# Kernel tuning notes

Hardware: AMD Instinct MI355X
Metric: run time of the kernel (lower is better)

## Reference

```python
import jax, jax.numpy as jnp
import numpy as np

EPS = 1e-9
TAU = 100.0
HX = 1.0
HY = 1.0


def _sym_pad(x):
    # torch Pad(1, padding_mode='symmetric') == numpy/jnp 'symmetric'
    return jnp.pad(x, ((0, 0), (0, 0), (1, 1), (1, 1)), mode='symmetric')


def _zero_interior(x):
    # zeroPadGS: keep interior, zero 1-px border
    return jnp.pad(x[:, :, 1:-1, 1:-1], ((0, 0), (0, 0), (1, 1), (1, 1)))


def _frob(x):
    # per-(batch,channel) Frobenius norm; only used in control-flow comparisons
    return jax.lax.stop_gradient(jnp.sqrt(jnp.sum(x * x, axis=(2, 3))))


def _apply_stencil(inp, boo, bmo, bom, bop, bpo):
    # applyStencilGS: mirror-pad interior, apply 5-point stencil, zero border
    p = _sym_pad(inp[:, :, 1:-1, 1:-1])
    res = (boo * p[:, :, 1:-1, 1:-1]
           + bmo * p[:, :, :-2, 1:-1]
           + bom * p[:, :, 1:-1, :-2]
           + bop * p[:, :, 1:-1, 2:]
           + bpo * p[:, :, 2:, 1:-1])
    return jnp.pad(res, ((0, 0), (0, 0), (1, 1), (1, 1)))


def _forward(V, mask1, mask2, kmax):
    B, C, nx0, ny0 = V.shape
    # U = per-image mean of V
    U = jnp.broadcast_to(jnp.mean(V, axis=(2, 3), keepdims=True), V.shape)
    Ut = jnp.swapaxes(_sym_pad(U), 2, 3)
    Vt = jnp.swapaxes(_sym_pad(V), 2, 3)
    m1 = jnp.swapaxes(_sym_pad(mask1), 2, 3)
    m2 = jnp.swapaxes(_sym_pad(mask2), 2, 3)
    nx, ny = ny0, nx0
    # drift vectors: forward difference / forward average (conv f1/f2, f3/f4)
    d1 = (Vt[:, :, 1:, :] - Vt[:, :, :-1, :]) / (HX * 0.5 * (Vt[:, :, 1:, :] + Vt[:, :, :-1, :]))
    d2 = (Vt[:, :, :, 1:] - Vt[:, :, :, :-1]) / (HY * 0.5 * (Vt[:, :, :, 1:] + Vt[:, :, :, :-1]))
    d1f = jnp.zeros_like(Vt).at[:, :, :nx + 1, 1:ny + 1].set(d1[:, :, :, 1:ny + 1]) * m1
    d2f = jnp.zeros_like(Vt).at[:, :, 1:nx + 1, :ny + 1].set(d2[:, :, 1:nx + 1, :]) * m2
    rx, ry = TAU / (2 * HX), TAU / (2 * HY)
    rxx, ryy = TAU / (HX * HX), TAU / (HY * HY)
    # conv 'same' with kernel [1,-1,0] (cross-correlation): out[i] = d[i-1] - d[i]
    c1 = jnp.pad(d1f, ((0, 0), (0, 0), (1, 0), (0, 0)))[:, :, :-1, :] - d1f
    c2 = jnp.pad(d2f, ((0, 0), (0, 0), (0, 0), (1, 0)))[:, :, :, :-1] - d2f
    boo_full = 1 + 2 * (rxx + ryy) - rx * c1 - ry * c2
    boo = boo_full[:, :, 1:nx + 1, 1:ny + 1]
    bpo = -rxx + rx * d1f[:, :, 1:nx + 1, 1:ny + 1]
    bop = -ryy + ry * d2f[:, :, 1:nx + 1, 1:ny + 1]
    bmo = -rxx - rx * d1f[:, :, :nx, 1:ny + 1]
    bom = -ryy - ry * d2f[:, :, 1:nx + 1, :ny]

    A = lambda z: _apply_stencil(z, boo, bmo, bom, bop, bpo)
    thresh = EPS * nx * ny
    x0 = Ut
    b = Ut
    p0 = _zero_interior(b - A(x0))
    r0_abs = _frob(p0)
    zc = jnp.zeros((B, C), dtype=V.dtype)
    zf = jnp.zeros_like(x0)
    k0 = jnp.zeros((B, C), dtype=jnp.int32)
    carry0 = (x0, p0, p0, zf, p0, zf, zf, zf, r0_abs, r0_abs, zc, zc, zc, zc, zc, k0)

    def step(carry, _):
        x, r, r_0, r_old, p, v, s, t, r_abs, r0_abs, sigma, alpha, omega, beta, v_abs, k = carry
        conv = (k < kmax) & (r_abs > thresh)
        convE = conv[:, :, None, None]
        v = jnp.where(convE, A(p), v)
        sigma = jnp.where(conv, jnp.sum(v * r_0, axis=(2, 3)), sigma)
        v_abs = jnp.where(conv, _frob(v), v_abs)
        res = sigma <= EPS * v_abs * r0_abs
        res1 = conv & res
        res1E = res1[:, :, None, None]
        p = jnp.where(res1E, _zero_interior(b - A(x)), p)
        r = jnp.where(res1E, p, r)
        r_0 = jnp.where(res1E, p, r_0)
        r0_abs = jnp.where(res1, _frob(r_0), r0_abs)
        r_abs = jnp.where(res1, r0_abs, r_abs)
        k = jnp.where(res1, k + 1, k)
        nres = conv & ~res
        nresE = nres[:, :, None, None]
        alpha = jnp.where(nres, jnp.sum(r * r_0, axis=(2, 3)) / jnp.where(nres, sigma, 1.0), alpha)
        s = jnp.where(nresE, r - alpha[:, :, None, None] * v, s)
        conv2 = _frob(s) <= thresh
        c3E = (nres & conv2)[:, :, None, None]
        x = jnp.where(c3E, x + alpha[:, :, None, None] * p, x)
        r = jnp.where(c3E, s, r)
        c4 = nres & ~conv2
        c4E = c4[:, :, None, None]
        t = jnp.where(c4E, A(s), t)
        omega = jnp.where(c4, jnp.sum(t * s, axis=(2, 3)) / jnp.where(c4, jnp.sum(t * t, axis=(2, 3)), 1.0), omega)
        x = jnp.where(c4E, x + alpha[:, :, None, None] * p + omega[:, :, None, None] * s, x)
        r_old = jnp.where(c4E, r, r_old)
        r = jnp.where(c4E, s - omega[:, :, None, None] * t, r)
        beta = jnp.where(c4, (alpha / jnp.where(c4, omega, 1.0)) * (jnp.sum(r * r_0, axis=(2, 3)) / jnp.where(c4, jnp.sum(r_old * r_0, axis=(2, 3)), 1.0)), beta)
        p = jnp.where(c4E, r + beta[:, :, None, None] * (p - omega[:, :, None, None] * v), p)
        k = jnp.where(nres, k + 1, k)
        r_abs = jnp.where(nres, _frob(r), r_abs)
        return (x, r, r_0, r_old, p, v, s, t, r_abs, r0_abs, sigma, alpha, omega, beta, v_abs, k), None

    carry, _ = jax.lax.scan(step, carry0, jnp.arange(kmax))
    return carry[0]


def setup_inputs() -> dict:
    key = jax.random.key(0)
    k1, k2, k3 = jax.random.split(key, 3)
    B, C, N = 8, 1, 512
    # strictly positive guidance image (V + offset in the original)
    V = jax.random.uniform(k1, (B, C, N, N), dtype=jnp.float32) * 0.99 + 0.005
    mask1 = (jax.random.uniform(k2, (B, C, N, N)) < 0.1).astype(jnp.float32)
    mask2 = (jax.random.uniform(k3, (B, C, N, N)) < 0.1).astype(jnp.float32)
    return {"V": V, "mask1": mask1, "mask2": mask2, "kmax": 16}


def reference(V, mask1, mask2, kmax):
    return _forward(V, mask1, mask2, kmax)
```

## Files before the change

kernel.cpp:

```cpp
#include <hip/hip_runtime.h>
#include <math.h>


namespace {

typedef unsigned long long ull;

constexpr int NIMG = 8;
constexpr int NSd  = 512;
constexpr int S    = NSd*NSd;
constexpr int NSF  = NIMG*S;
constexpr int PADS = 514;
constexpr int NB   = 256;
constexpr int IPB  = 32;
constexpr int NT   = 512;
constexpr float EPSF = 1e-9f;
constexpr float THR  = 1e-9f * 262144.0f;
constexpr float RX_=50.f, RY_=50.f, RXX_=100.f, RYY_=100.f;
constexpr float BOO0 = 1.f + 2.f*(RXX_+RYY_);

enum { P_PH=0, P_VH, P_TH, NPLH };
constexpr size_t A_QW = (size_t)NIMG*2*8*32;
constexpr size_t B_QW = (size_t)NIMG*2*8;

__device__ __forceinline__ int cl(int i){ return i<0?0:(i>NSd-1?NSd-1:i); }

#define LD4(d, p) { float4 _t4 = *reinterpret_cast<const float4*>(p); \
  (d)[0]=_t4.x; (d)[1]=_t4.y; (d)[2]=_t4.z; (d)[3]=_t4.w; }
#define ST4(p, s) { *reinterpret_cast<float4*>(p) = \
  make_float4((s)[0],(s)[1],(s)[2],(s)[3]); }
#define CP4(d, s) { (d)[0]=(s)[0]; (d)[1]=(s)[1]; (d)[2]=(s)[2]; (d)[3]=(s)[3]; }

#define LOADCOEF(rr_) \
  float ax[4], by[4], bym[4], axl; \
  LD4(ax, &axp[rr_][c4o]); \
  LD4(by, &byp[rr_][c4o]); \
  axl = __shfl_up(ax[3], 1); \
  if (lane==0) axl = c4o ? axp[rr_][c4o-1] : 0.f; \
  if ((rr_) > 0){ LD4(bym, &byp[(rr_)-1][c4o]); } else { CP4(bym, bym0_); }

__device__ __forceinline__ void hstore4(ull* pq, int off_f, const float s[4]){
  size_t q = (size_t)off_f >> 1;
  ull u0 = ((ull)__float_as_uint(s[1])<<32) | (ull)__float_as_uint(s[0]);
  ull u1 = ((ull)__float_as_uint(s[3])<<32) | (ull)__float_as_uint(s[2]);
  __hip_atomic_store(pq+q,   u0, __ATOMIC_RELAXED, __HIP_MEMORY_SCOPE_AGENT);
  __hip_atomic_store(pq+q+1, u1, __ATOMIC_RELAXED, __HIP_MEMORY_SCOPE_AGENT);
}
__device__ __forceinline__ void hload4(const ull* pq, int off_f, float d[4]){
  size_t q = (size_t)off_f >> 1;
  ull u0 = __hip_atomic_load(pq+q,   __ATOMIC_RELAXED, __HIP_MEMORY_SCOPE_AGENT);
  ull u1 = __hip_atomic_load(pq+q+1, __ATOMIC_RELAXED, __HIP_MEMORY_SCOPE_AGENT);
  d[0]=__uint_as_float((unsigned)u0); d[1]=__uint_as_float((unsigned)(u0>>32));
  d[2]=__uint_as_float((unsigned)u1); d[3]=__uint_as_float((unsigned)(u1>>32));
}

__device__ __forceinline__ void phase_sync(ull* Aq, ull* Bq, int img, int sub,
    unsigned ep, float* v, int n){
  __shared__ float acc[8][5];
  __shared__ float bc[5];
  const int tid = threadIdx.x, w = tid>>6, lane = tid&63;
  #pragma unroll
  for (int i=0;i<5;++i){
    if (i<n){
      float a = v[i];
      #pragma unroll
      for (int o=32;o;o>>=1) a += __shfl_xor(a,o);
      if (lane==0) acc[w][i] = a;
    }
  }
  __syncthreads();
  const int par = ep & 1;
  ull* Ab = Aq + ((size_t)(img*2+par)*8)*32;
  ull* Bb = Bq + ((size_t)(img*2+par))*8;
  if (sub == 0){
    if (w < n){
      float own = 0.f;
      #pragma unroll
      for (int i=0;i<8;++i) own += acc[i][w];
      ull x = 0; const bool me = (lane>=1 && lane<32);
      for(;;){
        bool ok = true;
        if (me){
          x = __hip_atomic_load(Ab + w*32 + lane, __ATOMIC_RELAXED, __HIP_MEMORY_SCOPE_AGENT);
          ok = ((unsigned)x == ep);
        }
        if (__all(ok)) break;
        __builtin_amdgcn_s_sleep(1);
      }
      float a = me ? __uint_as_float((unsigned)(x>>32)) : ((lane==0)? own : 0.f);
      #pragma unroll
      for (int o=16;o;o>>=1) a += __shfl_xor(a,o);
      if (lane==0){
        bc[w] = a;
        ull pk = ((ull)__float_as_uint(a)<<32) | (ull)ep;
        __hip_atomic_store(Bb + w, pk, __ATOMIC_RELAXED, __HIP_MEMORY_SCOPE_AGENT);
      }
    }
  } else {
    if (tid < n){
      float t = 0.f;
      #pragma unroll
      for (int i=0;i<8;++i) t += acc[i][tid];
      ull pk = ((ull)__float_as_uint(t)<<32) | (ull)ep;
      __hip_atomic_store(Ab + tid*32 + sub, pk, __ATOMIC_RELAXED, __HIP_MEMORY_SCOPE_AGENT);
    }
    if (w == 0){
      ull x = 0; const bool me = (lane < n);
      for(;;){
        bool ok = true;
        if (me){
          x = __hip_atomic_load(Bb + lane, __ATOMIC_RELAXED, __HIP_MEMORY_SCOPE_AGENT);
          ok = ((unsigned)x == ep);
        }
        if (__all(ok)) break;
        __builtin_amdgcn_s_sleep(1);
      }
      if (me) bc[lane] = __uint_as_float((unsigned)(x>>32));
    }
  }
  __syncthreads();
  #pragma unroll
  for (int i=0;i<5;++i) if (i<n) v[i] = bc[i];
}

__device__ __forceinline__ void stencil_reg(const float zc[4], float zl, float zr,
    const float zu[4], const float zd[4],
    const float ax[4], float axl, const float by[4], const float bym[4],
    float out[4]){
  #pragma unroll
  for (int j=0;j<4;++j){
    float axm = j ? ax[j-1] : axl;
    float zxm = j ? zc[j-1] : zl;
    float zxp = (j<3) ? zc[j+1] : zr;
    float boo = BOO0 + ax[j] - axm + by[j] - bym[j];
    out[j] = boo*zc[j] + (-RXX_-axm)*zxm + (-RYY_-bym[j])*zu[j]
           + (-RYY_+by[j])*zd[j] + (-RXX_+ax[j])*zxp;
  }
}

__global__ void __launch_bounds__(NT)
solve(const float* __restrict__ Vg,
    const float* __restrict__ M1g, const float* __restrict__ M2g,
    const int* __restrict__ kmp, float* __restrict__ outg, float* __restrict__ ws){
  __shared__ float tile[18][NSd];
  __shared__ float r0l[16][NSd];
  __shared__ float axp[16][NSd];
  __shared__ float byp[16][NSd];
  const int tid = threadIdx.x, blk = blockIdx.x;
  const int img = blk & 7, sub = blk >> 3;
  const int y0 = sub*16, bS = img*S;
  const int cg = tid & 127, r0b = tid >> 7, c4o = cg*4;
  const int lane = tid & 63;
  ull* PHq = (ull*)(ws + (size_t)P_PH*NSF);
  ull* VHq = (ull*)(ws + (size_t)P_VH*NSF);
  ull* THq = (ull*)(ws + (size_t)P_TH*NSF);
  ull* Aq  = (ull*)(ws + (size_t)NPLH*NSF);
  ull* Bq  = Aq + A_QW;
  unsigned ep = 0;
  const int kmax = kmp[0];
  const int row0o  = bS + (y0<<9) + c4o;
  const int row15o = bS + ((y0+15)<<9) + c4o;
  const int rowm1o = bS + ((y0-1)<<9) + c4o;
  const int row16o = bS + ((y0+16)<<9) + c4o;
  float red[5];

  float bym0_[4];
  float msum = 0.f;
  #pragma unroll
  for (int k=0;k<4;++k){
    int rr = 4*r0b + k, fy = y0 + rr, ro = bS + (fy<<9);
    float vc[4], vd[4], m1[4], m2[4], ca[4], cb[4];
    LD4(vc, Vg+ro+c4o);
    float vr  = Vg[ro + (c4o<508 ? c4o+4 : 511)];
    LD4(vd, Vg + bS + (cl(fy+1)<<9) + c4o);
    LD4(m1, M1g+ro+c4o);
    LD4(m2, M2g+ro+c4o);
    #pragma unroll
    for (int j=0;j<4;++j){
      float vn = (j<3) ? vc[j+1] : vr;
      ca[j] = RX_*((vn-vc[j])/(0.5f*(vn+vc[j])))*m1[j];
      cb[j] = RY_*((vd[j]-vc[j])/(0.5f*(vd[j]+vc[j])))*m2[j];
      msum += vc[j];
    }
    ST4(&axp[rr][c4o], ca);
    ST4(&byp[rr][c4o], cb);
  }
  if (r0b==0 && sub>0){
    int ro = bS + (y0<<9);
    float vc[4], vu[4], m2u[4];
    LD4(vc, Vg+ro+c4o);
    LD4(vu, Vg + bS + ((y0-1)<<9) + c4o);
    LD4(m2u, M2g + bS + ((y0-1)<<9) + c4o);
    #pragma unroll
    for (int j=0;j<4;++j)
      bym0_[j] = RY_*((vc[j]-vu[j])/(0.5f*(vc[j]+vu[j])))*m2u[j];
  } else {
    bym0_[0]=0.f; bym0_[1]=0.f; bym0_[2]=0.f; bym0_[3]=0.f;
  }
  red[0]=msum;
  ++ep; phase_sync(Aq,Bq,img,sub,ep, red, 1);
  const float c = red[0]*(1.0f/262144.0f);

  float x_[4][4], p_[4][4], r_[4][4], v_[4][4];
  float ph_[4], rh_[4], xh_[4], vh_[4];
  {
    float pa = 0.f;
    #pragma unroll
    for (int k=0;k<4;++k){
      int rr = 4*r0b + k;
      LOADCOEF(rr);
      float pn4[4];
      #pragma unroll
      for (int j=0;j<4;++j){
        float axm = j ? ax[j-1] : axl;
        float pn = -2.f*c*(ax[j]-axm + by[j]-bym[j]);
        x_[k][j]=c; p_[k][j]=pn; r_[k][j]=pn; v_[k][j]=0.f;
        pn4[j]=pn;
        pa += pn*pn;
      }
      ST4(&r0l[rr][c4o], pn4);
    }
    #pragma unroll
    for (int j=0;j<4;++j){ xh_[j]=c; ph_[j]=0.f; rh_[j]=0.f; vh_[j]=0.f; }
    if (r0b==0) hstore4(PHq, row0o, p_[0]);
    if (r0b==3) hstore4(PHq, row15o, p_[3]);
    red[0]=pa;
    ++ep; phase_sync(Aq,Bq,img,sub,ep, red, 1);
  }
  float rr0 = red[0];
  float r0abs = sqrtf(rr0), rabs = r0abs;
  int kcnt = 0;
  bool c4p = false;
  float alpha=0.f, omega=0.f, beta=0.f;

  for (int it=0; it<kmax; ++it){
    if (!((kcnt < kmax) && (rabs > THR))) break;

    if (c4p){
      #pragma unroll
      for (int k=0;k<4;++k)
        #pragma unroll
        for (int j=0;j<4;++j)
          p_[k][j] = r_[k][j] + beta*(p_[k][j]-omega*v_[k][j]);
      if (r0b==0 || r0b==3){
        #pragma unroll
        for (int j=0;j<4;++j) ph_[j] = rh_[j] + beta*(ph_[j]-omega*vh_[j]);
      }
    } else {
      if (r0b==0){
        if (sub==0){ CP4(ph_, p_[0]); } else hload4(PHq, rowm1o, ph_);
        CP4(rh_, ph_);
      }
      if (r0b==3){
        if (sub==IPB-1){ CP4(ph_, p_[3]); } else hload4(PHq, row16o, ph_);
        CP4(rh_, ph_);
      }
    }
    #pragma unroll
    for (int k=0;k<4;++k){ ST4(&tile[4*r0b+k+1][c4o], p_[k]); }
    if (r0b==0) ST4(&tile[0][c4o], ph_);
    if (r0b==3) ST4(&tile[17][c4o], ph_);
    __syncthreads();
    {
      float s1=0.f, s2=0.f;
      #pragma unroll
      for (int k=0;k<4;++k){
        int rr = 4*r0b+k, st = rr+1;
        LOADCOEF(rr);
        float zu[4], zd[4], ov[4], r0v[4];
        LD4(zu, &tile[st-1][c4o]);
        LD4(zd, &tile[st+1][c4o]);
        LD4(r0v, &r0l[rr][c4o]);
        float zl = __shfl_up(p_[k][3], 1);
        float zr = __shfl_down(p_[k][0], 1);
        if (lane==0)  zl = (c4o==0)   ? p_[k][0] : tile[st][c4o-1];
        if (lane==63) zr = (c4o==508) ? p_[k][3] : tile[st][c4o+4];
        stencil_reg(p_[k], zl, zr, zu, zd, ax, axl, by, bym, ov);
        #pragma unroll
        for (int j=0;j<4;++j){
          v_[k][j]=ov[j]; s1 += ov[j]*r0v[j]; s2 += ov[j]*ov[j];
        }
      }
      if (r0b==0) hstore4(VHq, row0o, v_[0]);
      if (r0b==3) hstore4(VHq, row15o, v_[3]);
      red[0]=s1; red[1]=s2;
      ++ep; phase_sync(Aq,Bq,img,sub,ep, red, 2);
    }
    float sig = red[0], vabs = sqrtf(red[1]);

    if (sig <= EPSF*vabs*r0abs){
      #pragma unroll
      for (int k=0;k<4;++k){ ST4(&tile[4*r0b+k+1][c4o], x_[k]); }
      if (r0b==0) ST4(&tile[0][c4o], xh_);
      if (r0b==3) ST4(&tile[17][c4o], xh_);
      __syncthreads();
      float pa = 0.f;
      #pragma unroll
      for (int k=0;k<4;++k){
        int rr = 4*r0b+k, st = rr+1;
        LOADCOEF(rr);
        float zu[4], zd[4], av[4], pn4[4];
        LD4(zu, &tile[st-1][c4o]);
        LD4(zd, &tile[st+1][c4o]);
        float zl = __shfl_up(x_[k][3], 1);
        float zr = __shfl_down(x_[k][0], 1);
        if (lane==0)  zl = (c4o==0)   ? x_[k][0] : tile[st][c4o-1];
        if (lane==63) zr = (c4o==508) ? x_[k][3] : tile[st][c4o+4];
        stencil_reg(x_[k], zl, zr, zu, zd, ax, axl, by, bym, av);
        #pragma unroll
        for (int j=0;j<4;++j){
          float pn = c - av[j];
          p_[k][j]=pn; r_[k][j]=pn; pn4[j]=pn;
          pa += pn*pn;
        }
        ST4(&r0l[rr][c4o], pn4);
      }
      if (r0b==0) hstore4(PHq, row0o, p_[0]);
      if (r0b==3) hstore4(PHq, row15o, p_[3]);
      red[0]=pa;
      ++ep; phase_sync(Aq,Bq,img,sub,ep, red, 1);
      rr0 = red[0]; r0abs = sqrtf(rr0); rabs = r0abs; kcnt++;
      c4p = false;
      continue;
    }

    alpha = rr0 / sig;
    if (r0b==0){
      if (sub==0){ CP4(vh_, v_[0]); } else hload4(VHq, rowm1o, vh_);
    }
    if (r0b==3){
      if (sub==IPB-1){ CP4(vh_, v_[3]); } else hload4(VHq, row16o, vh_);
    }
    {
      float tk[4][4];
      float ssp = 0.f;
      #pragma unroll
      for (int k=0;k<4;++k){
        float sv[4];
        #pragma unroll
        for (int j=0;j<4;++j){
          sv[j] = r_[k][j] - alpha*v_[k][j];
          ssp += sv[j]*sv[j];
        }
        ST4(&tile[4*r0b+k+1][c4o], sv);
      }
      if (r0b==0){
        float sh[4];
        #pragma unroll
        for (int j=0;j<4;++j) sh[j] = rh_[j] - alpha*vh_[j];
        ST4(&tile[0][c4o], sh);
      }
      if (r0b==3){
        float sh[4];
        #pragma unroll
        for (int j=0;j<4;++j) sh[j] = rh_[j] - alpha*vh_[j];
        ST4(&tile[17][c4o], sh);
      }
      __syncthreads();
      float tsp=0.f, ttp=0.f, sr0p=0.f, tr0p=0.f;
      #pragma unroll
      for (int k=0;k<4;++k){
        int rr = 4*r0b+k, st = rr+1;
        LOADCOEF(rr);
        float zc[4], zu[4], zd[4], tv[4], r0v[4];
        #pragma unroll
        for (int j=0;j<4;++j) zc[j] = r_[k][j] - alpha*v_[k][j];
        LD4(zu, &tile[st-1][c4o]);
        LD4(zd, &tile[st+1][c4o]);
        LD4(r0v, &r0l[rr][c4o]);
        float zl = __shfl_up(zc[3], 1);
        float zr = __shfl_down(zc[0], 1);
        if (lane==0)  zl = (c4o==0)   ? zc[0] : tile[st][c4o-1];
        if (lane==63) zr = (c4o==508) ? zc[3] : tile[st][c4o+4];
        stencil_reg(zc, zl, zr, zu, zd, ax, axl, by, bym, tv);
        #pragma unroll
        for (int j=0;j<4;++j){
          tsp  += tv[j]*zc[j];
          ttp  += tv[j]*tv[j];
          sr0p += zc[j]*r0v[j];
          tr0p += tv[j]*r0v[j];
        }
        CP4(tk[k], tv);
      }
      if (r0b==0) hstore4(THq, row0o, tk[0]);
      if (r0b==3) hstore4(THq, row15o, tk[3]);
      __syncthreads();
      #pragma unroll
      for (int k=0;k<4;++k){ ST4(&tile[4*r0b+k+1][c4o], tk[k]); }
      red[0]=ssp; red[1]=tsp; red[2]=ttp; red[3]=sr0p; red[4]=tr0p;
      ++ep; phase_sync(Aq,Bq,img,sub,ep, red, 5);
    }
    float ss=red[0], ts=red[1], tt=red[2], s_r0=red[3], t_r0=red[4];
    float snorm = sqrtf(ss);

    if (snorm <= THR){
      #pragma unroll
      for (int k=0;k<4;++k)
        #pragma unroll
        for (int j=0;j<4;++j) x_[k][j] += alpha*p_[k][j];
      rabs = snorm; kcnt++; c4p = false;
      continue;
    }

    omega = ts/tt;
    #pragma unroll
    for (int k=0;k<4;++k){
      int st = 4*r0b+k+1;
      float tv[4];
      LD4(tv, &tile[st][c4o]);
      #pragma unroll
      for (int j=0;j<4;++j){
        float sv = r_[k][j] - alpha*v_[k][j];
        x_[k][j] = x_[k][j] + alpha*p_[k][j] + omega*sv;
        r_[k][j] = sv - omega*tv[j];
      }
    }
    if (r0b==0){
      float th[4];
      if (sub==0){ LD4(th, &tile[1][c4o]); } else hload4(THq, rowm1o, th);
      #pragma unroll
      for (int j=0;j<4;++j){
        float sh = rh_[j] - alpha*vh_[j];
        xh_[j] = xh_[j] + alpha*ph_[j] + omega*sh;
        rh_[j] = sh - omega*th[j];
      }
    }
    if (r0b==3){
      float th[4];
      if (sub==IPB-1){ LD4(th, &tile[16][c4o]); } else hload4(THq, row16o, th);
      #pragma unroll
      for (int j=0;j<4;++j){
        float sh = rh_[j] - alpha*vh_[j];
        xh_[j] = xh_[j] + alpha*ph_[j] + omega*sh;
        rh_[j] = sh - omega*th[j];
      }
    }
    float rr0n = s_r0 - omega*t_r0;
    rabs = sqrtf(fmaxf(ss - 2.f*omega*ts + omega*omega*tt, 0.f));
    beta = alpha/omega*(rr0n/rr0);
    rr0 = rr0n; kcnt++;
    c4p = true;
  }

  __syncthreads();
  float* lp = &tile[0][0];
  #pragma unroll
  for (int k=0;k<4;++k){
    int ri = 4*r0b + k;
    ST4(lp + ri*516 + c4o, x_[k]);
  }
  float* outb = outg + (size_t)img*PADS*PADS;
  if (sub == 0){
    for (int e = tid; e < 2052; e += NT){
      int i, j;
      if (e < 514)      { i=0;        j=e;      }
      else if (e < 1028){ i=513;      j=e-514;  }
      else if (e < 1540){ i=e-1028+1; j=0;      }
      else              { i=e-1540+1; j=513;    }
      outb[i*PADS+j] = c;
    }
  }
  __syncthreads();
  {
    int qq = tid & 15, xb = tid >> 4;
    #pragma unroll
    for (int ps=0; ps<16; ++ps){
      int xc = ps*32 + xb;
      outb[(size_t)(xc+1)*PADS + (y0+1+qq)] = lp[qq*516 + xc];
    }
  }
}

}

extern "C" void kernel_launch(void* const* d_in, const int* in_sizes, int n_in,
                              void* d_out, int out_size, void* d_ws, size_t ws_size,
                              hipStream_t stream){
  const float* V  = (const float*)d_in[0];
  const float* M1 = (const float*)d_in[1];
  const float* M2 = (const float*)d_in[2];
  const int*   km = (const int*)d_in[3];
  float* ws  = (float*)d_ws;
  float* out = (float*)d_out;

  size_t need = (size_t)NPLH*NSF*sizeof(float) + (A_QW + B_QW)*sizeof(ull);
  if (ws_size < need) return;

  hipMemsetAsync((char*)d_ws + (size_t)NPLH*NSF*sizeof(float),
                 0, (A_QW + B_QW)*sizeof(ull), stream);

  solve<<<dim3(NB), dim3(NT), 0, stream>>>(V, M1, M2, km, out, ws);
}
```

Before: 217.3 us.

## Replace two-level leader barrier with all-to-all slot polling in phase sync

The per-image cross-block reduction used to have sub-block 0 gather the partial sums from the other 31 blocks and then broadcast the total through a second array. Now every block writes its partial sum to a slot, and each block polls all 32 slots and reduces them locally. This takes the leader round-trip (gather, then broadcast) off the critical path of each of the many syncs per iteration. In exchange, polling traffic on the shared slots rises, since all 32 blocks read every slot.

```diff
diff --git a/kernel.cpp b/kernel.cpp
--- a/kernel.cpp
+++ b/kernel.cpp
@@ -21,7 +21,6 @@
 
 enum { P_PH=0, P_VH, P_TH, NPLH };
 constexpr size_t A_QW = (size_t)NIMG*2*8*32;
-constexpr size_t B_QW = (size_t)NIMG*2*8;
 
 __device__ __forceinline__ int cl(int i){ return i<0?0:(i>NSd-1?NSd-1:i); }
 
@@ -54,7 +53,7 @@
   d[2]=__uint_as_float((unsigned)u1); d[3]=__uint_as_float((unsigned)(u1>>32));
 }
 
-__device__ __forceinline__ void phase_sync(ull* Aq, ull* Bq, int img, int sub,
+__device__ __forceinline__ void phase_sync(ull* Aq, int img, int sub,
     unsigned ep, float* v, int n){
   __shared__ float acc[8][5];
   __shared__ float bc[5];
@@ -69,54 +68,29 @@
     }
   }
   __syncthreads();
-  const int par = ep & 1;
-  ull* Ab = Aq + ((size_t)(img*2+par)*8)*32;
-  ull* Bb = Bq + ((size_t)(img*2+par))*8;
-  if (sub == 0){
-    if (w < n){
-      float own = 0.f;
-      #pragma unroll
-      for (int i=0;i<8;++i) own += acc[i][w];
-      ull x = 0; const bool me = (lane>=1 && lane<32);
-      for(;;){
-        bool ok = true;
-        if (me){
-          x = __hip_atomic_load(Ab + w*32 + lane, __ATOMIC_RELAXED, __HIP_MEMORY_SCOPE_AGENT);
-          ok = ((unsigned)x == ep);
-        }
-        if (__all(ok)) break;
-        __builtin_amdgcn_s_sleep(1);
-      }
-      float a = me ? __uint_as_float((unsigned)(x>>32)) : ((lane==0)? own : 0.f);
-      #pragma unroll
-      for (int o=16;o;o>>=1) a += __shfl_xor(a,o);
-      if (lane==0){
-        bc[w] = a;
-        ull pk = ((ull)__float_as_uint(a)<<32) | (ull)ep;
-        __hip_atomic_store(Bb + w, pk, __ATOMIC_RELAXED, __HIP_MEMORY_SCOPE_AGENT);
-      }
-    }
-  } else {
-    if (tid < n){
-      float t = 0.f;
-      #pragma unroll
-      for (int i=0;i<8;++i) t += acc[i][tid];
-      ull pk = ((ull)__float_as_uint(t)<<32) | (ull)ep;
-      __hip_atomic_store(Ab + tid*32 + sub, pk, __ATOMIC_RELAXED, __HIP_MEMORY_SCOPE_AGENT);
-    }
-    if (w == 0){
-      ull x = 0; const bool me = (lane < n);
-      for(;;){
-        bool ok = true;
-        if (me){
-          x = __hip_atomic_load(Bb + lane, __ATOMIC_RELAXED, __HIP_MEMORY_SCOPE_AGENT);
-          ok = ((unsigned)x == ep);
-        }
-        if (__all(ok)) break;
-        __builtin_amdgcn_s_sleep(1);
-      }
-      if (me) bc[lane] = __uint_as_float((unsigned)(x>>32));
-    }
+  ull* Ab = Aq + ((size_t)(img*2+(int)(ep&1u))*8)*32;
+  if (tid < n){
+    float t = 0.f;
+    #pragma unroll
+    for (int i=0;i<8;++i) t += acc[i][tid];
+    ull pk = ((ull)__float_as_uint(t)<<32) | (ull)ep;
+    __hip_atomic_store(Ab + tid*32 + sub, pk, __ATOMIC_RELAXED, __HIP_MEMORY_SCOPE_AGENT);
+  }
+  if (w < n){
+    ull x = 0; const bool me = (lane < 32);
+    for(;;){
+      bool ok = true;
+      if (me){
+        x = __hip_atomic_load(Ab + w*32 + lane, __ATOMIC_RELAXED, __HIP_MEMORY_SCOPE_AGENT);
+        ok = ((unsigned)x == ep);
+      }
+      if (__all(ok)) break;
+      __builtin_amdgcn_s_sleep(1);
+    }
+    float a = me ? __uint_as_float((unsigned)(x>>32)) : 0.f;
+    #pragma unroll
+    for (int o=16;o;o>>=1) a += __shfl_xor(a,o);
+    if (lane==0) bc[w] = a;
   }
   __syncthreads();
   #pragma unroll
@@ -155,7 +129,6 @@
   ull* VHq = (ull*)(ws + (size_t)P_VH*NSF);
   ull* THq = (ull*)(ws + (size_t)P_TH*NSF);
   ull* Aq  = (ull*)(ws + (size_t)NPLH*NSF);
-  ull* Bq  = Aq + A_QW;
   unsigned ep = 0;
   const int kmax = kmp[0];
   const int row0o  = bS + (y0<<9) + c4o;
@@ -198,7 +171,7 @@
     bym0_[0]=0.f; bym0_[1]=0.f; bym0_[2]=0.f; bym0_[3]=0.f;
   }
   red[0]=msum;
-  ++ep; phase_sync(Aq,Bq,img,sub,ep, red, 1);
+  ++ep; phase_sync(Aq,img,sub,ep, red, 1);
   const float c = red[0]*(1.0f/262144.0f);
 
   float x_[4][4], p_[4][4], r_[4][4], v_[4][4];
@@ -225,7 +198,7 @@
     if (r0b==0) hstore4(PHq, row0o, p_[0]);
     if (r0b==3) hstore4(PHq, row15o, p_[3]);
     red[0]=pa;
-    ++ep; phase_sync(Aq,Bq,img,sub,ep, red, 1);
+    ++ep; phase_sync(Aq,img,sub,ep, red, 1);
   }
   float rr0 = red[0];
   float r0abs = sqrtf(rr0), rabs = r0abs;
@@ -284,7 +257,7 @@
       if (r0b==0) hstore4(VHq, row0o, v_[0]);
       if (r0b==3) hstore4(VHq, row15o, v_[3]);
       red[0]=s1; red[1]=s2;
-      ++ep; phase_sync(Aq,Bq,img,sub,ep, red, 2);
+      ++ep; phase_sync(Aq,img,sub,ep, red, 2);
     }
     float sig = red[0], vabs = sqrtf(red[1]);
 
@@ -318,7 +291,7 @@
       if (r0b==0) hstore4(PHq, row0o, p_[0]);
       if (r0b==3) hstore4(PHq, row15o, p_[3]);
       red[0]=pa;
-      ++ep; phase_sync(Aq,Bq,img,sub,ep, red, 1);
+      ++ep; phase_sync(Aq,img,sub,ep, red, 1);
       rr0 = red[0]; r0abs = sqrtf(rr0); rabs = r0abs; kcnt++;
       c4p = false;
       continue;
@@ -388,7 +361,7 @@
       #pragma unroll
       for (int k=0;k<4;++k){ ST4(&tile[4*r0b+k+1][c4o], tk[k]); }
       red[0]=ssp; red[1]=tsp; red[2]=ttp; red[3]=sr0p; red[4]=tr0p;
-      ++ep; phase_sync(Aq,Bq,img,sub,ep, red, 5);
+      ++ep; phase_sync(Aq,img,sub,ep, red, 5);
     }
     float ss=red[0], ts=red[1], tt=red[2], s_r0=red[3], t_r0=red[4];
     float snorm = sqrtf(ss);
@@ -483,11 +456,11 @@
   float* ws  = (float*)d_ws;
   float* out = (float*)d_out;
 
-  size_t need = (size_t)NPLH*NSF*sizeof(float) + (A_QW + B_QW)*sizeof(ull);
+  size_t need = (size_t)NPLH*NSF*sizeof(float) + A_QW*sizeof(ull);
   if (ws_size < need) return;
 
   hipMemsetAsync((char*)d_ws + (size_t)NPLH*NSF*sizeof(float),
-                 0, (A_QW + B_QW)*sizeof(ull), stream);
+                 0, A_QW*sizeof(ull), stream);
 
   solve<<<dim3(NB), dim3(NT), 0, stream>>>(V, M1, M2, km, out, ws);
 }
```

New measurement: 252.1 us. +16.0%, slower.
